# Kernel optimization log

Hardware: AMD Instinct MI355X
Metric: run time of the kernel (lower is better)

## Reference

```python
import jax, jax.numpy as jnp
import numpy as np

NUM_HEADS = 64
HEAD_DIM = 10  # forced by nn.Linear(10, 1)


def setup_inputs() -> dict:
    key = jax.random.key(0)
    kq, kk, kv, kw = jax.random.split(key, 4)
    B, T, M = 16, 4096, NUM_HEADS * HEAD_DIM
    return {
        "query": jax.random.normal(kq, (B, T, M), dtype=jnp.float32),
        "key": jax.random.normal(kk, (B, T, M), dtype=jnp.float32),
        "value": jax.random.normal(kv, (B, T, M), dtype=jnp.float32),
        "W": jax.random.normal(kw, (1, HEAD_DIM), dtype=jnp.float32) * 0.3,
        "b": jnp.zeros((1,), dtype=jnp.float32),
    }


def _to_heads(x):
    # torch: stack(split(x, head_dim, dim=2), dim=0) -> [H, B, T, D]
    B, T, M = x.shape
    return x.reshape(B, T, NUM_HEADS, HEAD_DIM).transpose(2, 0, 1, 3)


def reference(query, key, value, W, b):
    D = HEAD_DIM
    q = _to_heads(query)   # [H,B,T,D]
    k = _to_heads(key)     # [H,B,T,D]
    v = _to_heads(value)   # [H,B,T,D]
    # key.transpose(-1,-2).sum(3).unsqueeze(2): sum over T -> [H,B,1,D]
    k_sum = k.sum(axis=2, keepdims=True)
    attn = jax.nn.softmax(jnp.tanh(q * k_sum / np.float32(np.sqrt(D))), axis=-1)
    t = attn * v                          # [H,B,T,D]
    v_q = t.sum(axis=2)                   # [H,B,D]
    v_v = t.sum(axis=3).transpose(1, 0, 2)  # [B,H,T]
    # input_proj: Linear(10,1) on v_q*v_q (v_query == v_key == t summed over T)
    s = jnp.tanh((v_q * v_q) @ W.T + b)   # [H,B,1]
    s = jax.nn.softmax(s, axis=-1)        # softmax over size-1 dim (== ones)
    s = s.transpose(1, 0, 2)              # [B,H,1]
    return v_v * s                        # [B,H,T]
```

## Files before the change

### kernel.cpp

```cpp
#include <hip/hip_runtime.h>
#include <stdint.h>

#define BB 16
#define TT 4096
#define HH 64
#define MM 640

#define ROWS 4
#define TILE_F4 (ROWS * 160)

__global__ void __launch_bounds__(256)
ksum_kernel(const float* __restrict__ key, float* __restrict__ ksum) {
    int g = blockIdx.x * blockDim.x + threadIdx.x;
    int b = g / 160;
    int c = g % 160;
    int t0 = blockIdx.y * 32;

    const float4* p = reinterpret_cast<const float4*>(key)
                    + (size_t)b * TT * 160 + (size_t)t0 * 160 + c;

    float4 a0 = make_float4(0.f,0.f,0.f,0.f);
    float4 a1 = make_float4(0.f,0.f,0.f,0.f);
    float4 a2 = make_float4(0.f,0.f,0.f,0.f);
    float4 a3 = make_float4(0.f,0.f,0.f,0.f);
    #pragma unroll
    for (int i = 0; i < 32; i += 4) {
        float4 x0 = p[(size_t)(i + 0) * 160];
        float4 x1 = p[(size_t)(i + 1) * 160];
        float4 x2 = p[(size_t)(i + 2) * 160];
        float4 x3 = p[(size_t)(i + 3) * 160];
        a0.x += x0.x; a0.y += x0.y; a0.z += x0.z; a0.w += x0.w;
        a1.x += x1.x; a1.y += x1.y; a1.z += x1.z; a1.w += x1.w;
        a2.x += x2.x; a2.y += x2.y; a2.z += x2.z; a2.w += x2.w;
        a3.x += x3.x; a3.y += x3.y; a3.z += x3.z; a3.w += x3.w;
    }
    float sx = (a0.x + a1.x) + (a2.x + a3.x);
    float sy = (a0.y + a1.y) + (a2.y + a3.y);
    float sz = (a0.z + a1.z) + (a2.z + a3.z);
    float sw = (a0.w + a1.w) + (a2.w + a3.w);

    float* dst = ksum + b * MM + c * 4;
    atomicAdd(dst + 0, sx);
    atomicAdd(dst + 1, sy);
    atomicAdd(dst + 2, sz);
    atomicAdd(dst + 3, sw);
}

__device__ __forceinline__ float tanh_rcp(float x) {
    float ax = fabsf(x);
    float e2 = __expf(-2.0f * ax);
    float th = (1.0f - e2) * __builtin_amdgcn_rcpf(1.0f + e2);
    return copysignf(th, x);
}

__global__ void __launch_bounds__(256)
attn_kernel(const float* __restrict__ q,
            const float* __restrict__ v,
            const float* __restrict__ ksum,
            float* __restrict__ out) {
    __shared__ float4 s4[2 * TILE_F4];

    const int tid = threadIdx.x;
    const int t0  = blockIdx.x * ROWS;
    const int b   = blockIdx.y;

    const int row  = tid >> 6;
    const int head = tid & 63;

    const float R = 0.316227766016838f;
    float ksr[10];
    {
        const float* ks = ksum + b * MM + head * 10;
        #pragma unroll
        for (int d = 0; d < 10; ++d) ksr[d] = ks[d] * R;
    }

    const float4* qt = (const float4*)q + ((size_t)b * TT + t0) * 160;
    const float4* vt = (const float4*)v + ((size_t)b * TT + t0) * 160;

    float4 rs[5];
    #pragma unroll
    for (int i = 0; i < 5; ++i) {
        int idx = tid + 256 * i;
        rs[i] = (idx < 640) ? qt[idx] : vt[idx - 640];
    }
    #pragma unroll
    for (int i = 0; i < 5; ++i)
        s4[tid + 256 * i] = rs[i];
    __syncthreads();

    const float* qf = reinterpret_cast<const float*>(s4);
    const int base = row * MM + head * 10;

    float sum = 0.f, dot = 0.f;
    #pragma unroll
    for (int d = 0; d < 10; ++d) {
        float e = __expf(tanh_rcp(qf[base + d] * ksr[d]));
        sum += e;
        dot += e * qf[2560 + base + d];
    }
    out[((size_t)(b * HH + head)) * TT + t0 + row]
        = dot * __builtin_amdgcn_rcpf(sum);
}

extern "C" void kernel_launch(void* const* d_in, const int* in_sizes, int n_in,
                              void* d_out, int out_size, void* d_ws, size_t ws_size,
                              hipStream_t stream) {
    const float* q = (const float*)d_in[0];
    const float* k = (const float*)d_in[1];
    const float* v = (const float*)d_in[2];
    float* out  = (float*)d_out;
    float* ksum = (float*)d_ws;

    hipMemsetAsync(d_ws, 0, (size_t)BB * MM * sizeof(float), stream);
    ksum_kernel<<<dim3(10, 128), dim3(256), 0, stream>>>(k, ksum);
    attn_kernel<<<dim3(TT / ROWS, BB), dim3(256), 0, stream>>>(q, v, ksum, out);
}
```

Measured before the change: 131.3 us.

## Retile attention kernel by head groups with padded LDS and XCD-aware block swizzle

The attention kernel is retiled so each 128-thread block covers 16 time rows and a 16-head group, with each thread producing two heads. Q and V tiles go into separate LDS buffers with a padded row stride to reduce bank conflicts, and the ksum loads become float2. Both kernels now run on a 1D grid with a modulo-8 block-index swizzle, which looks aimed at keeping neighbouring tiles on the same XCD/L2. The cost is more index arithmetic and global reads of 160-byte segments per row instead of whole contiguous rows.

```diff
diff --git a/kernel.cpp b/kernel.cpp
--- a/kernel.cpp
+++ b/kernel.cpp
@@ -6,15 +6,20 @@
 #define HH 64
 #define MM 640
 
-#define ROWS 4
-#define TILE_F4 (ROWS * 160)
+#define TROWS 16
+#define PADF4 41
 
 __global__ void __launch_bounds__(256)
 ksum_kernel(const float* __restrict__ key, float* __restrict__ ksum) {
-    int g = blockIdx.x * blockDim.x + threadIdx.x;
+    int i   = blockIdx.x;
+    int swz = (i & 7) * 160 + (i >> 3);
+    int cx  = swz % 10;
+    int ty  = swz / 10;
+
+    int g = cx * 256 + threadIdx.x;
     int b = g / 160;
     int c = g % 160;
-    int t0 = blockIdx.y * 32;
+    int t0 = ty * 32;
 
     const float4* p = reinterpret_cast<const float4*>(key)
                     + (size_t)b * TT * 160 + (size_t)t0 * 160 + c;
@@ -24,11 +29,11 @@
     float4 a2 = make_float4(0.f,0.f,0.f,0.f);
     float4 a3 = make_float4(0.f,0.f,0.f,0.f);
     #pragma unroll
-    for (int i = 0; i < 32; i += 4) {
-        float4 x0 = p[(size_t)(i + 0) * 160];
-        float4 x1 = p[(size_t)(i + 1) * 160];
-        float4 x2 = p[(size_t)(i + 2) * 160];
-        float4 x3 = p[(size_t)(i + 3) * 160];
+    for (int j = 0; j < 32; j += 4) {
+        float4 x0 = p[(size_t)(j + 0) * 160];
+        float4 x1 = p[(size_t)(j + 1) * 160];
+        float4 x2 = p[(size_t)(j + 2) * 160];
+        float4 x3 = p[(size_t)(j + 3) * 160];
         a0.x += x0.x; a0.y += x0.y; a0.z += x0.z; a0.w += x0.w;
         a1.x += x1.x; a1.y += x1.y; a1.z += x1.z; a1.w += x1.w;
         a2.x += x2.x; a2.y += x2.y; a2.z += x2.z; a2.w += x2.w;
@@ -53,54 +58,77 @@
     return copysignf(th, x);
 }
 
-__global__ void __launch_bounds__(256)
+__global__ void __launch_bounds__(128)
 attn_kernel(const float* __restrict__ q,
             const float* __restrict__ v,
             const float* __restrict__ ksum,
             float* __restrict__ out) {
-    __shared__ float4 s4[2 * TILE_F4];
+    __shared__ float qs[TROWS * PADF4 * 4];
+    __shared__ float vs[TROWS * PADF4 * 4];
 
     const int tid = threadIdx.x;
-    const int t0  = blockIdx.x * ROWS;
-    const int b   = blockIdx.y;
 
-    const int row  = tid >> 6;
-    const int head = tid & 63;
+    int i   = blockIdx.x;
+    int swz = (i & 7) * 2048 + (i >> 3);
+    const int hg = swz & 3;
+    const int t0 = ((swz >> 2) & 255) * TROWS;
+    const int b  = swz >> 10;
+
+    const float4* qg = reinterpret_cast<const float4*>(q)
+                     + ((size_t)(b * TT + t0)) * 160 + hg * 40;
+    const float4* vg = reinterpret_cast<const float4*>(v)
+                     + ((size_t)(b * TT + t0)) * 160 + hg * 40;
+
+    float4 rq[5], rv[5];
+    #pragma unroll
+    for (int j = 0; j < 5; ++j) {
+        int idx = tid + 128 * j;
+        int row = idx / 40;
+        int c   = idx % 40;
+        rq[j] = qg[(size_t)row * 160 + c];
+        rv[j] = vg[(size_t)row * 160 + c];
+    }
+    float4* qs4 = reinterpret_cast<float4*>(qs);
+    float4* vs4 = reinterpret_cast<float4*>(vs);
+    #pragma unroll
+    for (int j = 0; j < 5; ++j) {
+        int idx = tid + 128 * j;
+        int row = idx / 40;
+        int c   = idx % 40;
+        qs4[row * PADF4 + c] = rq[j];
+        vs4[row * PADF4 + c] = rv[j];
+    }
+    __syncthreads();
 
     const float R = 0.316227766016838f;
-    float ksr[10];
-    {
-        const float* ks = ksum + b * MM + head * 10;
-        #pragma unroll
-        for (int d = 0; d < 10; ++d) ksr[d] = ks[d] * R;
+    const int head0 = tid >> 4;
+    const int row   = tid & 15;
+
+    const float* ks0 = ksum + b * MM + hg * 160 + head0 * 10;
+    const float* ks1 = ks0 + 80;
+    float2 kk0[5], kk1[5];
+    #pragma unroll
+    for (int j = 0; j < 5; ++j) {
+        kk0[j] = *reinterpret_cast<const float2*>(ks0 + 2 * j);
+        kk1[j] = *reinterpret_cast<const float2*>(ks1 + 2 * j);
     }
 
-    const float4* qt = (const float4*)q + ((size_t)b * TT + t0) * 160;
-    const float4* vt = (const float4*)v + ((size_t)b * TT + t0) * 160;
-
-    float4 rs[5];
     #pragma unroll
-    for (int i = 0; i < 5; ++i) {
-        int idx = tid + 256 * i;
-        rs[i] = (idx < 640) ? qt[idx] : vt[idx - 640];
+    for (int o = 0; o < 2; ++o) {
+        const int head  = head0 + o * 8;
+        const int lbase = row * (PADF4 * 4) + head * 10;
+        const float2* kk = o ? kk1 : kk0;
+        float sum = 0.f, dot = 0.f;
+        #pragma unroll
+        for (int j = 0; j < 5; ++j) {
+            float e0 = __expf(tanh_rcp(qs[lbase + 2*j]     * kk[j].x * R));
+            float e1 = __expf(tanh_rcp(qs[lbase + 2*j + 1] * kk[j].y * R));
+            sum += e0 + e1;
+            dot += e0 * vs[lbase + 2*j] + e1 * vs[lbase + 2*j + 1];
+        }
+        out[((size_t)(b * HH + hg * 16 + head)) * TT + t0 + row]
+            = dot * __builtin_amdgcn_rcpf(sum);
     }
-    #pragma unroll
-    for (int i = 0; i < 5; ++i)
-        s4[tid + 256 * i] = rs[i];
-    __syncthreads();
-
-    const float* qf = reinterpret_cast<const float*>(s4);
-    const int base = row * MM + head * 10;
-
-    float sum = 0.f, dot = 0.f;
-    #pragma unroll
-    for (int d = 0; d < 10; ++d) {
-        float e = __expf(tanh_rcp(qf[base + d] * ksr[d]));
-        sum += e;
-        dot += e * qf[2560 + base + d];
-    }
-    out[((size_t)(b * HH + head)) * TT + t0 + row]
-        = dot * __builtin_amdgcn_rcpf(sum);
 }
 
 extern "C" void kernel_launch(void* const* d_in, const int* in_sizes, int n_in,
@@ -113,6 +141,6 @@
     float* ksum = (float*)d_ws;
 
     hipMemsetAsync(d_ws, 0, (size_t)BB * MM * sizeof(float), stream);
-    ksum_kernel<<<dim3(10, 128), dim3(256), 0, stream>>>(k, ksum);
-    attn_kernel<<<dim3(TT / ROWS, BB), dim3(256), 0, stream>>>(q, v, ksum, out);
+    ksum_kernel<<<dim3(1280), dim3(256), 0, stream>>>(k, ksum);
+    attn_kernel<<<dim3(16384), dim3(128), 0, stream>>>(q, v, ksum, out);
 }
```

Result: faster. 116.1 us (-11.6%).

## Load head pairs directly into registers with float4, drop shared-memory staging

Applied to the files above, without the earlier changes.

The attention kernel no longer stages q and v tiles through shared memory behind a barrier. Each thread now handles two adjacent heads (20 floats) for one token and loads q, v and the key sums straight into registers with float4 loads. The launch becomes a flat 1D grid of 8192 blocks. The aim is to remove the LDS round trip and the __syncthreads, at the cost of per-thread strided global loads (80-byte spans) that coalesce less well and output stores that are scattered across rows TT apart.

```diff
diff --git a/kernel.cpp b/kernel.cpp
--- a/kernel.cpp
+++ b/kernel.cpp
@@ -5,9 +5,6 @@
 #define TT 4096
 #define HH 64
 #define MM 640
-
-#define ROWS 4
-#define TILE_F4 (ROWS * 160)
 
 __global__ void __launch_bounds__(256)
 ksum_kernel(const float* __restrict__ key, float* __restrict__ ksum) {
@@ -58,49 +55,48 @@
             const float* __restrict__ v,
             const float* __restrict__ ksum,
             float* __restrict__ out) {
-    __shared__ float4 s4[2 * TILE_F4];
+    const int u  = blockIdx.x * 256 + threadIdx.x;
+    const int hp = u & 31;
+    const int t  = (u >> 5) & (TT - 1);
+    const int b  = u >> 17;
 
-    const int tid = threadIdx.x;
-    const int t0  = blockIdx.x * ROWS;
-    const int b   = blockIdx.y;
+    const float4* qp = reinterpret_cast<const float4*>(
+        q + ((size_t)b * TT + t) * MM + hp * 20);
+    const float4* vp = reinterpret_cast<const float4*>(
+        v + ((size_t)b * TT + t) * MM + hp * 20);
+    const float4* kp = reinterpret_cast<const float4*>(
+        ksum + (size_t)b * MM + hp * 20);
 
-    const int row  = tid >> 6;
-    const int head = tid & 63;
+    float4 rq[5], rv[5], rk[5];
+    #pragma unroll
+    for (int j = 0; j < 5; ++j) rq[j] = qp[j];
+    #pragma unroll
+    for (int j = 0; j < 5; ++j) rv[j] = vp[j];
+    #pragma unroll
+    for (int j = 0; j < 5; ++j) rk[j] = kp[j];
 
+    const float* qf = reinterpret_cast<const float*>(rq);
+    const float* vf = reinterpret_cast<const float*>(rv);
+    const float* kf = reinterpret_cast<const float*>(rk);
     const float R = 0.316227766016838f;
-    float ksr[10];
-    {
-        const float* ks = ksum + b * MM + head * 10;
+
+    float res[2];
+    #pragma unroll
+    for (int h = 0; h < 2; ++h) {
+        float sum = 0.f, dot = 0.f;
         #pragma unroll
-        for (int d = 0; d < 10; ++d) ksr[d] = ks[d] * R;
+        for (int d = 0; d < 10; ++d) {
+            int j = h * 10 + d;
+            float e = __expf(tanh_rcp(qf[j] * kf[j] * R));
+            sum += e;
+            dot += e * vf[j];
+        }
+        res[h] = dot * __builtin_amdgcn_rcpf(sum);
     }
 
-    const float4* qt = (const float4*)q + ((size_t)b * TT + t0) * 160;
-    const float4* vt = (const float4*)v + ((size_t)b * TT + t0) * 160;
-
-    float4 rs[5];
-    #pragma unroll
-    for (int i = 0; i < 5; ++i) {
-        int idx = tid + 256 * i;
-        rs[i] = (idx < 640) ? qt[idx] : vt[idx - 640];
-    }
-    #pragma unroll
-    for (int i = 0; i < 5; ++i)
-        s4[tid + 256 * i] = rs[i];
-    __syncthreads();
-
-    const float* qf = reinterpret_cast<const float*>(s4);
-    const int base = row * MM + head * 10;
-
-    float sum = 0.f, dot = 0.f;
-    #pragma unroll
-    for (int d = 0; d < 10; ++d) {
-        float e = __expf(tanh_rcp(qf[base + d] * ksr[d]));
-        sum += e;
-        dot += e * qf[2560 + base + d];
-    }
-    out[((size_t)(b * HH + head)) * TT + t0 + row]
-        = dot * __builtin_amdgcn_rcpf(sum);
+    float* ob = out + ((size_t)(b * HH + hp * 2)) * TT + t;
+    ob[0]  = res[0];
+    ob[TT] = res[1];
 }
 
 extern "C" void kernel_launch(void* const* d_in, const int* in_sizes, int n_in,
@@ -114,5 +110,5 @@
 
     hipMemsetAsync(d_ws, 0, (size_t)BB * MM * sizeof(float), stream);
     ksum_kernel<<<dim3(10, 128), dim3(256), 0, stream>>>(k, ksum);
-    attn_kernel<<<dim3(TT / ROWS, BB), dim3(256), 0, stream>>>(q, v, ksum, out);
+    attn_kernel<<<dim3(8192), dim3(256), 0, stream>>>(q, v, ksum, out);
 }
```

New measurement: 140.6 us. 1.07x slower.

## Persistent per-wave loop with register prefetch and LDS-transposed float4 output stores

Applied to the files above, without the earlier changes.

Restructures the attention kernel so that each wavefront handles 16 timesteps in a loop. It prefetches the next pair of q/v rows into registers while computing the current pair, with no block-level syncs. Results are staged in LDS and transposed so each lane writes contiguous float4 runs along T instead of scattered scalar stores. The grid shrinks to 1024 blocks, which cuts launch count and output write inefficiency but lowers parallelism and may limit memory-level concurrency.

```diff
diff --git a/kernel.cpp b/kernel.cpp
--- a/kernel.cpp
+++ b/kernel.cpp
@@ -5,9 +5,6 @@
 #define TT 4096
 #define HH 64
 #define MM 640
-
-#define ROWS 4
-#define TILE_F4 (ROWS * 160)
 
 __global__ void __launch_bounds__(256)
 ksum_kernel(const float* __restrict__ key, float* __restrict__ ksum) {
@@ -58,49 +55,102 @@
             const float* __restrict__ v,
             const float* __restrict__ ksum,
             float* __restrict__ out) {
-    __shared__ float4 s4[2 * TILE_F4];
+    __shared__ float4 lds4[4][640];
 
-    const int tid = threadIdx.x;
-    const int t0  = blockIdx.x * ROWS;
-    const int b   = blockIdx.y;
-
-    const int row  = tid >> 6;
-    const int head = tid & 63;
+    const int tid  = threadIdx.x;
+    const int w    = tid >> 6;
+    const int lane = tid & 63;
+    const int part = blockIdx.x & 63;
+    const int b    = blockIdx.x >> 6;
 
     const float R = 0.316227766016838f;
     float ksr[10];
     {
-        const float* ks = ksum + b * MM + head * 10;
+        const float* ks = ksum + b * MM + lane * 10;
         #pragma unroll
         for (int d = 0; d < 10; ++d) ksr[d] = ks[d] * R;
     }
 
-    const float4* qt = (const float4*)q + ((size_t)b * TT + t0) * 160;
-    const float4* vt = (const float4*)v + ((size_t)b * TT + t0) * 160;
+    const float4* q4 = (const float4*)q + (size_t)b * TT * 160;
+    const float4* v4 = (const float4*)v + (size_t)b * TT * 160;
 
-    float4 rs[5];
+    float4* qb = &lds4[w][0];
+    float4* vb = &lds4[w][320];
+    const float* qf = (const float*)qb;
+    const float* vf = (const float*)vb;
+
+    const int T0 = part * 32 + w * 8;
+    float  oacc[16];
+    float4 rq[5], rv[5];
+
+    {
+        size_t g = (size_t)(T0 * 2) * 160;
+        #pragma unroll
+        for (int j = 0; j < 5; ++j) {
+            rq[j] = q4[g + lane + 64 * j];
+            rv[j] = v4[g + lane + 64 * j];
+        }
+        #pragma unroll
+        for (int j = 0; j < 5; ++j) {
+            qb[lane + 64 * j] = rq[j];
+            vb[lane + 64 * j] = rv[j];
+        }
+    }
+
     #pragma unroll
-    for (int i = 0; i < 5; ++i) {
-        int idx = tid + 256 * i;
-        rs[i] = (idx < 640) ? qt[idx] : vt[idx - 640];
+    for (int i = 0; i < 8; ++i) {
+        if (i < 7) {
+            size_t g = (size_t)((T0 + i + 1) * 2) * 160;
+            #pragma unroll
+            for (int j = 0; j < 5; ++j) {
+                rq[j] = q4[g + lane + 64 * j];
+                rv[j] = v4[g + lane + 64 * j];
+            }
+        }
+        __builtin_amdgcn_sched_barrier(0);
+
+        #pragma unroll
+        for (int r = 0; r < 2; ++r) {
+            const int fb = r * 640 + lane * 10;
+            float sum = 0.f, dot = 0.f;
+            #pragma unroll
+            for (int d = 0; d < 10; ++d) {
+                float e = __expf(tanh_rcp(qf[fb + d] * ksr[d]));
+                sum += e;
+                dot += e * vf[fb + d];
+            }
+            oacc[i * 2 + r] = dot * __builtin_amdgcn_rcpf(sum);
+        }
+        __builtin_amdgcn_sched_barrier(0);
+
+        if (i < 7) {
+            #pragma unroll
+            for (int j = 0; j < 5; ++j) {
+                qb[lane + 64 * j] = rq[j];
+                vb[lane + 64 * j] = rv[j];
+            }
+        }
     }
+
+    float* tb = (float*)qb;
     #pragma unroll
-    for (int i = 0; i < 5; ++i)
-        s4[tid + 256 * i] = rs[i];
-    __syncthreads();
+    for (int s = 0; s < 16; ++s)
+        tb[s * 64 + lane] = oacc[s];
 
-    const float* qf = reinterpret_cast<const float*>(s4);
-    const int base = row * MM + head * 10;
-
-    float sum = 0.f, dot = 0.f;
+    const int tw0 = part * 64 + w * 16;
+    float* ob = out + (size_t)b * HH * TT;
     #pragma unroll
-    for (int d = 0; d < 10; ++d) {
-        float e = __expf(tanh_rcp(qf[base + d] * ksr[d]));
-        sum += e;
-        dot += e * qf[2560 + base + d];
+    for (int j = 0; j < 4; ++j) {
+        int s  = j * 64 + lane;
+        int h  = s >> 2;
+        int t4 = (s & 3) * 4;
+        float4 o;
+        o.x = tb[(t4 + 0) * 64 + h];
+        o.y = tb[(t4 + 1) * 64 + h];
+        o.z = tb[(t4 + 2) * 64 + h];
+        o.w = tb[(t4 + 3) * 64 + h];
+        *(float4*)(ob + (size_t)h * TT + tw0 + t4) = o;
     }
-    out[((size_t)(b * HH + head)) * TT + t0 + row]
-        = dot * __builtin_amdgcn_rcpf(sum);
 }
 
 extern "C" void kernel_launch(void* const* d_in, const int* in_sizes, int n_in,
@@ -114,5 +164,5 @@
 
     hipMemsetAsync(d_ws, 0, (size_t)BB * MM * sizeof(float), stream);
     ksum_kernel<<<dim3(10, 128), dim3(256), 0, stream>>>(k, ksum);
-    attn_kernel<<<dim3(TT / ROWS, BB), dim3(256), 0, stream>>>(q, v, ksum, out);
+    attn_kernel<<<dim3(BB * 64), dim3(256), 0, stream>>>(q, v, ksum, out);
 }
```

New measurement: 166.0 us. 1.26x slower.
